# Optimization experiments

Hardware: AMD Instinct MI355X
Metric: run time of the kernel (lower is better)

The kernel has to match this reference:

```python
import jax, jax.numpy as jnp
import numpy as np

IGNORE_INDEX = -100


def setup_inputs() -> dict:
    key = jax.random.key(0)
    k1, k2, k3 = jax.random.split(key, 3)
    B, S, D, V = 4, 2048, 2048, 32000
    outputs = jax.random.normal(k1, (B, S, D), dtype=jnp.float32)
    W = jax.random.normal(k2, (V, D), dtype=jnp.float32) * (D ** -0.5)
    targets = jax.random.randint(k3, (B, S), 0, V, dtype=jnp.int64)
    return {"outputs": outputs, "W": W, "targets": targets}


def reference(outputs, W, targets):
    # outputs: [B, S, D], W: [V, D], targets: [B, S]
    B, S, D = outputs.shape
    h = outputs.reshape(-1, D)                      # [N, D], N = B*S
    t = targets.reshape(-1)                         # [N]
    mask = t != IGNORE_INDEX                        # [N] bool
    # Linear projection to vocab logits (fp32 CE as in original).
    logits = jnp.einsum("nd,vd->nv", h, W).astype(jnp.float32)  # [N, V]
    logp = jax.nn.log_softmax(logits, axis=-1)      # [N, V]
    t_safe = jnp.where(mask, t, 0)
    nll = -jnp.take_along_axis(logp, t_safe[:, None], axis=1)[:, 0]  # [N]
    loss_sum = jnp.sum(jnp.where(mask, nll, 0.0))
    num_valid = jnp.sum(mask).astype(jnp.float32)
    return jnp.where(num_valid > 0, loss_sum / num_valid, loss_sum)
```

## Files before the change

kernel.cpp:

```cpp
#include <hip/hip_runtime.h>
#include <hip/hip_bf16.h>

#define IGNORE_INDEX (-100)

constexpr int Nrows = 8192;
constexpr int Dk    = 2048;
constexpr int Vv    = 32000;

constexpr int BK8  = 128;
constexpr int NKT8 = Dk / BK8;
constexpr int NT   = Vv / 128;
constexpr int NTP  = 256;

typedef __attribute__((ext_vector_type(8))) short   short8;
typedef __attribute__((ext_vector_type(8))) __bf16  bf16x8;
typedef __attribute__((ext_vector_type(4))) float   f32x4;
typedef __attribute__((ext_vector_type(8))) int     i32x8;

typedef const __attribute__((address_space(1))) void* gptr_t;
typedef __attribute__((address_space(3))) void*       lptr_t;

static __device__ __forceinline__ unsigned pack_bf16x2(float x, float y) {
    __hip_bfloat162 h = __float22bfloat162_rn(make_float2(x, y));
    unsigned u;
    __builtin_memcpy(&u, &h, 4);
    return u;
}

static __device__ __forceinline__ i32x8 mk8(uint4 lo, uint4 hi) {
    i32x8 v;
    v[0] = lo.x; v[1] = lo.y; v[2] = lo.z; v[3] = lo.w;
    v[4] = hi.x; v[5] = hi.y; v[6] = hi.z; v[7] = hi.w;
    return v;
}

__global__ __launch_bounds__(256)
void lce_cast_fp8(const float* __restrict__ src, unsigned char* __restrict__ dst,
                  float mul, int n16) {
    int i = blockIdx.x * blockDim.x + threadIdx.x;
    const int stride = gridDim.x * blockDim.x;
    for (; i < n16; i += stride) {
        const float4* s = (const float4*)src + (size_t)i * 4;
        unsigned w[4];
        #pragma unroll
        for (int j = 0; j < 4; ++j) {
            float4 f = s[j];
            int t0 = __builtin_amdgcn_cvt_pk_fp8_f32(f.x * mul, f.y * mul, 0, false);
            t0 = __builtin_amdgcn_cvt_pk_fp8_f32(f.z * mul, f.w * mul, t0, true);
            w[j] = (unsigned)t0;
        }
        ((uint4*)dst)[i] = make_uint4(w[0], w[1], w[2], w[3]);
    }
}

__global__ __launch_bounds__(256, 4)
void lce_gemm_lse_fp8(const unsigned char* __restrict__ ax,
                      const unsigned char* __restrict__ bx,
                      float* __restrict__ pmax, float* __restrict__ psum) {
    __shared__ __align__(16) unsigned char As[128 * 128];
    __shared__ __align__(16) unsigned char Bs[128 * 128];
    __shared__ float redmax[128][2];
    __shared__ float redsum[128][2];

    const int t    = threadIdx.x;
    const int lane = t & 63;
    const int wid  = t >> 6;
    const int wrow = wid >> 1;
    const int wcol = wid & 1;
    const int l15  = lane & 15;
    const int l4   = lane >> 4;

    const int rowBase = blockIdx.x * 128;
    const int colBase = blockIdx.y * 128;

    f32x4 acc[4][4] = {};

    for (int kt = 0; kt < NKT8; ++kt) {
        const int kg = kt * BK8;
        #pragma unroll
        for (int r = 0; r < 4; ++r) {
            const int c   = r * 256 + t;
            const int row = c >> 3;
            const int e   = (c & 7) ^ (row & 7);
            const int gu  = ((e & 3) << 1) | (e >> 2);
            __builtin_amdgcn_global_load_lds(
                (gptr_t)(ax + (size_t)(rowBase + row) * Dk + kg + gu * 16),
                (lptr_t)&As[(r * 256 + wid * 64) * 16], 16, 0, 0);
        }
        #pragma unroll
        for (int r = 0; r < 4; ++r) {
            const int c   = r * 256 + t;
            const int row = c >> 3;
            const int e   = (c & 7) ^ (row & 7);
            const int gu  = ((e & 3) << 1) | (e >> 2);
            __builtin_amdgcn_global_load_lds(
                (gptr_t)(bx + (size_t)(colBase + row) * Dk + kg + gu * 16),
                (lptr_t)&Bs[(r * 256 + wid * 64) * 16], 16, 0, 0);
        }
        __syncthreads();

        i32x8 av[4], bv[4];
        #pragma unroll
        for (int m = 0; m < 4; ++m) {
            const int row = wrow * 64 + m * 16 + l15;
            const int o0  = row * 128 + ((l4 ^ (row & 7)) * 16);
            uint4 lo = *(const uint4*)&As[o0];
            uint4 hi = *(const uint4*)&As[o0 ^ 64];
            av[m] = mk8(lo, hi);
        }
        #pragma unroll
        for (int n = 0; n < 4; ++n) {
            const int row = wcol * 64 + n * 16 + l15;
            const int o0  = row * 128 + ((l4 ^ (row & 7)) * 16);
            uint4 lo = *(const uint4*)&Bs[o0];
            uint4 hi = *(const uint4*)&Bs[o0 ^ 64];
            bv[n] = mk8(lo, hi);
        }
        #pragma unroll
        for (int m = 0; m < 4; ++m)
            #pragma unroll
            for (int n = 0; n < 4; ++n)
                acc[m][n] = __builtin_amdgcn_mfma_scale_f32_16x16x128_f8f6f4(
                    av[m], bv[n], acc[m][n], 0, 0,
                    0, 0x7F7F7F7F, 0, 0x79797979);
        __syncthreads();
    }

    float wmax[4][4];
    #pragma unroll
    for (int m = 0; m < 4; ++m) {
        #pragma unroll
        for (int r = 0; r < 4; ++r) {
            float v = fmaxf(fmaxf(acc[m][0][r], acc[m][1][r]),
                            fmaxf(acc[m][2][r], acc[m][3][r]));
            v = fmaxf(v, __shfl_xor(v, 1));
            v = fmaxf(v, __shfl_xor(v, 2));
            v = fmaxf(v, __shfl_xor(v, 4));
            v = fmaxf(v, __shfl_xor(v, 8));
            wmax[m][r] = v;
        }
    }
    if (l15 == 0) {
        #pragma unroll
        for (int m = 0; m < 4; ++m)
            #pragma unroll
            for (int r = 0; r < 4; ++r)
                redmax[wrow * 64 + m * 16 + l4 * 4 + r][wcol] = wmax[m][r];
    }
    __syncthreads();

    #pragma unroll
    for (int m = 0; m < 4; ++m) {
        #pragma unroll
        for (int r = 0; r < 4; ++r) {
            const int row = wrow * 64 + m * 16 + l4 * 4 + r;
            const float M = fmaxf(redmax[row][0], redmax[row][1]);
            float s = __expf(acc[m][0][r] - M) + __expf(acc[m][1][r] - M)
                    + __expf(acc[m][2][r] - M) + __expf(acc[m][3][r] - M);
            s += __shfl_xor(s, 1);
            s += __shfl_xor(s, 2);
            s += __shfl_xor(s, 4);
            s += __shfl_xor(s, 8);
            if (l15 == 0) redsum[row][wcol] = s;
        }
    }
    __syncthreads();

    if (wcol == 0 && l15 == 0) {
        #pragma unroll
        for (int m = 0; m < 4; ++m)
            #pragma unroll
            for (int r = 0; r < 4; ++r) {
                const int row = wrow * 64 + m * 16 + l4 * 4 + r;
                const float M = fmaxf(redmax[row][0], redmax[row][1]);
                const float S = redsum[row][0] + redsum[row][1];
                const size_t o = (size_t)(rowBase + row) * NTP + blockIdx.y;
                pmax[o] = M;
                psum[o] = S;
            }
    }
}

__global__ __launch_bounds__(256, 2)
void lce_gemm_lse_f32(const float* __restrict__ hx, const float* __restrict__ wx,
                      float* __restrict__ pmax, float* __restrict__ psum) {
    __shared__ unsigned short As[128 * 64];
    __shared__ unsigned short Bs[128 * 64];
    __shared__ float redmax[128][2];
    __shared__ float redsum[128][2];

    const int t    = threadIdx.x;
    const int lane = t & 63;
    const int wid  = t >> 6;
    const int wrow = wid >> 1;
    const int wcol = wid & 1;
    const int l15  = lane & 15;
    const int l4   = lane >> 4;

    const int rowBase = blockIdx.x * 128;
    const int colBase = blockIdx.y * 128;

    f32x4 acc[4][4] = {};

    const int srow   = t >> 3;
    const int schunk = t & 7;

    for (int kt = 0; kt < Dk / 64; ++kt) {
        const int kg = kt * 64 + schunk * 8;
        #pragma unroll
        for (int r = 0; r < 4; ++r) {
            const int row = srow + r * 32;
            const float* src = hx + (size_t)(rowBase + row) * Dk + kg;
            float4 f0 = *(const float4*)(src);
            float4 f1 = *(const float4*)(src + 4);
            const int off = row * 64 + ((schunk ^ (row & 7)) << 3);
            *(uint4*)(&As[off]) = make_uint4(
                pack_bf16x2(f0.x, f0.y), pack_bf16x2(f0.z, f0.w),
                pack_bf16x2(f1.x, f1.y), pack_bf16x2(f1.z, f1.w));
        }
        #pragma unroll
        for (int r = 0; r < 4; ++r) {
            const int row = srow + r * 32;
            const float* src = wx + (size_t)(colBase + row) * Dk + kg;
            float4 f0 = *(const float4*)(src);
            float4 f1 = *(const float4*)(src + 4);
            const int off = row * 64 + ((schunk ^ (row & 7)) << 3);
            *(uint4*)(&Bs[off]) = make_uint4(
                pack_bf16x2(f0.x, f0.y), pack_bf16x2(f0.z, f0.w),
                pack_bf16x2(f1.x, f1.y), pack_bf16x2(f1.z, f1.w));
        }
        __syncthreads();

        #pragma unroll
        for (int ks = 0; ks < 2; ++ks) {
            bf16x8 av[4], bv[4];
            const int unit = ks * 4 + l4;
            #pragma unroll
            for (int m = 0; m < 4; ++m) {
                const int row = wrow * 64 + m * 16 + l15;
                const int off = row * 64 + ((unit ^ (row & 7)) << 3);
                av[m] = __builtin_bit_cast(bf16x8, *(const short8*)(&As[off]));
            }
            #pragma unroll
            for (int n = 0; n < 4; ++n) {
                const int row = wcol * 64 + n * 16 + l15;
                const int off = row * 64 + ((unit ^ (row & 7)) << 3);
                bv[n] = __builtin_bit_cast(bf16x8, *(const short8*)(&Bs[off]));
            }
            #pragma unroll
            for (int m = 0; m < 4; ++m)
                #pragma unroll
                for (int n = 0; n < 4; ++n)
                    acc[m][n] = __builtin_amdgcn_mfma_f32_16x16x32_bf16(
                        av[m], bv[n], acc[m][n], 0, 0, 0);
        }
        __syncthreads();
    }

    float wmax[4][4];
    #pragma unroll
    for (int m = 0; m < 4; ++m) {
        #pragma unroll
        for (int r = 0; r < 4; ++r) {
            float v = fmaxf(fmaxf(acc[m][0][r], acc[m][1][r]),
                            fmaxf(acc[m][2][r], acc[m][3][r]));
            v = fmaxf(v, __shfl_xor(v, 1));
            v = fmaxf(v, __shfl_xor(v, 2));
            v = fmaxf(v, __shfl_xor(v, 4));
            v = fmaxf(v, __shfl_xor(v, 8));
            wmax[m][r] = v;
        }
    }
    if (l15 == 0) {
        #pragma unroll
        for (int m = 0; m < 4; ++m)
            #pragma unroll
            for (int r = 0; r < 4; ++r)
                redmax[wrow * 64 + m * 16 + l4 * 4 + r][wcol] = wmax[m][r];
    }
    __syncthreads();

    #pragma unroll
    for (int m = 0; m < 4; ++m) {
        #pragma unroll
        for (int r = 0; r < 4; ++r) {
            const int row = wrow * 64 + m * 16 + l4 * 4 + r;
            const float M = fmaxf(redmax[row][0], redmax[row][1]);
            float s = __expf(acc[m][0][r] - M) + __expf(acc[m][1][r] - M)
                    + __expf(acc[m][2][r] - M) + __expf(acc[m][3][r] - M);
            s += __shfl_xor(s, 1);
            s += __shfl_xor(s, 2);
            s += __shfl_xor(s, 4);
            s += __shfl_xor(s, 8);
            if (l15 == 0) redsum[row][wcol] = s;
        }
    }
    __syncthreads();

    if (wcol == 0 && l15 == 0) {
        #pragma unroll
        for (int m = 0; m < 4; ++m)
            #pragma unroll
            for (int r = 0; r < 4; ++r) {
                const int row = wrow * 64 + m * 16 + l4 * 4 + r;
                const float M = fmaxf(redmax[row][0], redmax[row][1]);
                const float S = redsum[row][0] + redsum[row][1];
                const size_t o = (size_t)(rowBase + row) * NTP + blockIdx.y;
                pmax[o] = M;
                psum[o] = S;
            }
    }
}

__global__ __launch_bounds__(256)
void lce_combine(const float* __restrict__ hx, const float* __restrict__ wx,
                 const int* __restrict__ tgt,
                 const float* __restrict__ pmax, const float* __restrict__ psum,
                 float* __restrict__ nll, int ntiles, int ntp) {
    const int row  = (blockIdx.x * blockDim.x + threadIdx.x) >> 6;
    const int lane = threadIdx.x & 63;
    if (row >= Nrows) return;

    float m = -INFINITY, s = 0.0f;
    for (int ti = lane; ti < ntiles; ti += 64) {
        const float pm = pmax[(size_t)row * ntp + ti];
        const float ps = psum[(size_t)row * ntp + ti];
        const float nm = fmaxf(m, pm);
        s = s * __expf(m - nm) + ps * __expf(pm - nm);
        m = nm;
    }
    #pragma unroll
    for (int d = 1; d < 64; d <<= 1) {
        const float om = __shfl_xor(m, d);
        const float os = __shfl_xor(s, d);
        const float nm = fmaxf(m, om);
        s = s * __expf(m - nm) + os * __expf(om - nm);
        m = nm;
    }
    const float lse = m + __logf(s);

    const int tg = tgt[row];
    const bool valid = (tg != IGNORE_INDEX);
    const int tw = valid ? tg : 0;
    const float* hr = hx + (size_t)row * Dk;
    const float* wr = wx + (size_t)tw * Dk;
    float acc = 0.0f;
    #pragma unroll
    for (int i = 0; i < 8; ++i) {
        const int off = lane * 4 + i * 256;
        float4 a = *(const float4*)(hr + off);
        float4 b = *(const float4*)(wr + off);
        acc += a.x * b.x + a.y * b.y + a.z * b.z + a.w * b.w;
    }
    #pragma unroll
    for (int d = 1; d < 64; d <<= 1) acc += __shfl_xor(acc, d);

    if (lane == 0) nll[row] = valid ? (lse - acc) : 0.0f;
}

__global__ __launch_bounds__(1024)
void lce_finalize(const float* __restrict__ nll, const int* __restrict__ tgt,
                  float* __restrict__ out) {
    __shared__ float ssum[1024];
    __shared__ float scnt[1024];
    const int t = threadIdx.x;
    float s = 0.0f, c = 0.0f;
    for (int i = t; i < Nrows; i += 1024) {
        s += nll[i];
        c += (tgt[i] != IGNORE_INDEX) ? 1.0f : 0.0f;
    }
    ssum[t] = s;
    scnt[t] = c;
    __syncthreads();
    for (int d = 512; d > 0; d >>= 1) {
        if (t < d) { ssum[t] += ssum[t + d]; scnt[t] += scnt[t + d]; }
        __syncthreads();
    }
    if (t == 0) out[0] = (scnt[0] > 0.0f) ? ssum[0] / scnt[0] : ssum[0];
}

extern "C" void kernel_launch(void* const* d_in, const int* in_sizes, int n_in,
                              void* d_out, int out_size, void* d_ws, size_t ws_size,
                              hipStream_t stream) {
    const float* hx  = (const float*)d_in[0];
    const float* wx  = (const float*)d_in[1];
    const int*   tgt = (const int*)d_in[2];
    float* out = (float*)d_out;

    float* pmax = (float*)d_ws;
    float* psum = pmax + (size_t)Nrows * NTP;
    float* nll  = psum + (size_t)Nrows * NTP;
    unsigned char* hq = (unsigned char*)(nll + Nrows);
    unsigned char* wq = hq + (size_t)Nrows * Dk;

    const size_t need = (size_t)Nrows * NTP * 8 + (size_t)Nrows * 4
                      + (size_t)Nrows * Dk + (size_t)Vv * Dk;

    if (ws_size >= need) {
        lce_cast_fp8<<<2048, 256, 0, stream>>>(hx, hq, 1.0f, Nrows * Dk / 16);
        lce_cast_fp8<<<2048, 256, 0, stream>>>(wx, wq, 64.0f, Vv * Dk / 16);
        lce_gemm_lse_fp8<<<dim3(Nrows / 128, NT), 256, 0, stream>>>(hq, wq, pmax, psum);
    } else {
        lce_gemm_lse_f32<<<dim3(Nrows / 128, NT), 256, 0, stream>>>(hx, wx, pmax, psum);
    }
    lce_combine<<<dim3((Nrows * 64) / 256), 256, 0, stream>>>(
        hx, wx, tgt, pmax, psum, nll, NT, NTP);
    lce_finalize<<<1, 1024, 0, stream>>>(nll, tgt, out);
}
```

Measured before the change: 656.6 us.

## Quantize GEMM operands to FP4 e2m1 instead of FP8 for logits

```diff
diff --git a/kernel.cpp b/kernel.cpp
--- a/kernel.cpp
+++ b/kernel.cpp
@@ -7,8 +7,7 @@
 constexpr int Dk    = 2048;
 constexpr int Vv    = 32000;
 
-constexpr int BK8  = 128;
-constexpr int NKT8 = Dk / BK8;
+constexpr int NKT4 = Dk / 128;
 constexpr int NT   = Vv / 128;
 constexpr int NTP  = 256;
 
@@ -27,38 +26,60 @@
     return u;
 }
 
-static __device__ __forceinline__ i32x8 mk8(uint4 lo, uint4 hi) {
+static __device__ __forceinline__ i32x8 mk4z(uint4 d) {
     i32x8 v;
-    v[0] = lo.x; v[1] = lo.y; v[2] = lo.z; v[3] = lo.w;
-    v[4] = hi.x; v[5] = hi.y; v[6] = hi.z; v[7] = hi.w;
+    v[0] = d.x; v[1] = d.y; v[2] = d.z; v[3] = d.w;
+    v[4] = 0;   v[5] = 0;   v[6] = 0;   v[7] = 0;
     return v;
 }
 
+static __device__ __forceinline__ unsigned q4(float x) {
+    const unsigned s = (__builtin_bit_cast(unsigned, x) >> 31) << 3;
+    const float a = fabsf(x);
+    unsigned c;
+    c = a < 0.25f ? 0u
+      : a < 0.75f ? 1u
+      : a < 1.25f ? 2u
+      : a < 1.75f ? 3u
+      : a < 2.5f  ? 4u
+      : a < 3.5f  ? 5u
+      : a < 5.0f  ? 6u : 7u;
+    return s | c;
+}
+
 __global__ __launch_bounds__(256)
-void lce_cast_fp8(const float* __restrict__ src, unsigned char* __restrict__ dst,
-                  float mul, int n16) {
+void lce_cast_fp4(const float* __restrict__ src, unsigned char* __restrict__ dst,
+                  float mul, int n32) {
     int i = blockIdx.x * blockDim.x + threadIdx.x;
     const int stride = gridDim.x * blockDim.x;
-    for (; i < n16; i += stride) {
-        const float4* s = (const float4*)src + (size_t)i * 4;
+    for (; i < n32; i += stride) {
+        const float4* s = (const float4*)src + (size_t)i * 8;
         unsigned w[4];
         #pragma unroll
         for (int j = 0; j < 4; ++j) {
-            float4 f = s[j];
-            int t0 = __builtin_amdgcn_cvt_pk_fp8_f32(f.x * mul, f.y * mul, 0, false);
-            t0 = __builtin_amdgcn_cvt_pk_fp8_f32(f.z * mul, f.w * mul, t0, true);
-            w[j] = (unsigned)t0;
+            float4 f0 = s[2 * j];
+            float4 f1 = s[2 * j + 1];
+            unsigned u = 0;
+            u |= q4(f0.x * mul);
+            u |= q4(f0.y * mul) << 4;
+            u |= q4(f0.z * mul) << 8;
+            u |= q4(f0.w * mul) << 12;
+            u |= q4(f1.x * mul) << 16;
+            u |= q4(f1.y * mul) << 20;
+            u |= q4(f1.z * mul) << 24;
+            u |= q4(f1.w * mul) << 28;
+            w[j] = u;
         }
         ((uint4*)dst)[i] = make_uint4(w[0], w[1], w[2], w[3]);
     }
 }
 
 __global__ __launch_bounds__(256, 4)
-void lce_gemm_lse_fp8(const unsigned char* __restrict__ ax,
+void lce_gemm_lse_fp4(const unsigned char* __restrict__ ax,
                       const unsigned char* __restrict__ bx,
                       float* __restrict__ pmax, float* __restrict__ psum) {
-    __shared__ __align__(16) unsigned char As[128 * 128];
-    __shared__ __align__(16) unsigned char Bs[128 * 128];
+    __shared__ __align__(16) unsigned char As[128 * 64];
+    __shared__ __align__(16) unsigned char Bs[128 * 64];
     __shared__ float redmax[128][2];
     __shared__ float redsum[128][2];
 
@@ -73,56 +94,50 @@
     const int rowBase = blockIdx.x * 128;
     const int colBase = blockIdx.y * 128;
 
+    const int RowB = Dk / 2;
+
     f32x4 acc[4][4] = {};
 
-    for (int kt = 0; kt < NKT8; ++kt) {
-        const int kg = kt * BK8;
-        #pragma unroll
-        for (int r = 0; r < 4; ++r) {
+    for (int kt = 0; kt < NKT4; ++kt) {
+        const int kg = kt * 64;
+        #pragma unroll
+        for (int r = 0; r < 2; ++r) {
             const int c   = r * 256 + t;
-            const int row = c >> 3;
-            const int e   = (c & 7) ^ (row & 7);
-            const int gu  = ((e & 3) << 1) | (e >> 2);
+            const int row = c >> 2;
+            const int gu  = (c & 3) ^ ((row >> 1) & 3);
             __builtin_amdgcn_global_load_lds(
-                (gptr_t)(ax + (size_t)(rowBase + row) * Dk + kg + gu * 16),
+                (gptr_t)(ax + (size_t)(rowBase + row) * RowB + kg + gu * 16),
                 (lptr_t)&As[(r * 256 + wid * 64) * 16], 16, 0, 0);
         }
         #pragma unroll
-        for (int r = 0; r < 4; ++r) {
+        for (int r = 0; r < 2; ++r) {
             const int c   = r * 256 + t;
-            const int row = c >> 3;
-            const int e   = (c & 7) ^ (row & 7);
-            const int gu  = ((e & 3) << 1) | (e >> 2);
+            const int row = c >> 2;
+            const int gu  = (c & 3) ^ ((row >> 1) & 3);
             __builtin_amdgcn_global_load_lds(
-                (gptr_t)(bx + (size_t)(colBase + row) * Dk + kg + gu * 16),
+                (gptr_t)(bx + (size_t)(colBase + row) * RowB + kg + gu * 16),
                 (lptr_t)&Bs[(r * 256 + wid * 64) * 16], 16, 0, 0);
         }
         __syncthreads();
 
-        i32x8 av[4], bv[4];
+        i32x8 bv[4];
+        #pragma unroll
+        for (int n = 0; n < 4; ++n) {
+            const int row = wcol * 64 + n * 16 + l15;
+            const int su  = l4 ^ ((row >> 1) & 3);
+            bv[n] = mk4z(*(const uint4*)&Bs[row * 64 + su * 16]);
+        }
         #pragma unroll
         for (int m = 0; m < 4; ++m) {
             const int row = wrow * 64 + m * 16 + l15;
-            const int o0  = row * 128 + ((l4 ^ (row & 7)) * 16);
-            uint4 lo = *(const uint4*)&As[o0];
-            uint4 hi = *(const uint4*)&As[o0 ^ 64];
-            av[m] = mk8(lo, hi);
-        }
-        #pragma unroll
-        for (int n = 0; n < 4; ++n) {
-            const int row = wcol * 64 + n * 16 + l15;
-            const int o0  = row * 128 + ((l4 ^ (row & 7)) * 16);
-            uint4 lo = *(const uint4*)&Bs[o0];
-            uint4 hi = *(const uint4*)&Bs[o0 ^ 64];
-            bv[n] = mk8(lo, hi);
-        }
-        #pragma unroll
-        for (int m = 0; m < 4; ++m)
+            const int su  = l4 ^ ((row >> 1) & 3);
+            i32x8 av = mk4z(*(const uint4*)&As[row * 64 + su * 16]);
             #pragma unroll
             for (int n = 0; n < 4; ++n)
                 acc[m][n] = __builtin_amdgcn_mfma_scale_f32_16x16x128_f8f6f4(
-                    av[m], bv[n], acc[m][n], 0, 0,
+                    av, bv[n], acc[m][n], 4, 4,
                     0, 0x7F7F7F7F, 0, 0x79797979);
+        }
         __syncthreads();
     }
 
@@ -391,15 +406,15 @@
     float* psum = pmax + (size_t)Nrows * NTP;
     float* nll  = psum + (size_t)Nrows * NTP;
     unsigned char* hq = (unsigned char*)(nll + Nrows);
-    unsigned char* wq = hq + (size_t)Nrows * Dk;
+    unsigned char* wq = hq + (size_t)Nrows * Dk / 2;
 
     const size_t need = (size_t)Nrows * NTP * 8 + (size_t)Nrows * 4
-                      + (size_t)Nrows * Dk + (size_t)Vv * Dk;
+                      + ((size_t)Nrows * Dk + (size_t)Vv * Dk) / 2;
 
     if (ws_size >= need) {
-        lce_cast_fp8<<<2048, 256, 0, stream>>>(hx, hq, 1.0f, Nrows * Dk / 16);
-        lce_cast_fp8<<<2048, 256, 0, stream>>>(wx, wq, 64.0f, Vv * Dk / 16);
-        lce_gemm_lse_fp8<<<dim3(Nrows / 128, NT), 256, 0, stream>>>(hq, wq, pmax, psum);
+        lce_cast_fp4<<<2048, 256, 0, stream>>>(hx, hq, 1.0f, Nrows * Dk / 32);
+        lce_cast_fp4<<<2048, 256, 0, stream>>>(wx, wq, 64.0f, Vv * Dk / 32);
+        lce_gemm_lse_fp4<<<dim3(Nrows / 128, NT), 256, 0, stream>>>(hq, wq, pmax, psum);
     } else {
         lce_gemm_lse_f32<<<dim3(Nrows / 128, NT), 256, 0, stream>>>(hx, wx, pmax, psum);
     }
```

New measurement: 530.5 us, median of 2. 1.24x faster.
